# Performance work log

Measured on AMD Instinct MI355X. Metric: run time of the kernel, lower is better.

Reference implementation:

```python
import jax, jax.numpy as jnp
import numpy as np

EMBED_DIM = 1024
NUM_HEADS = 16
HEAD_DIM = EMBED_DIM // NUM_HEADS


def setup_inputs() -> dict:
    key = jax.random.key(0)
    kx, kq, kk, kv, ko = jax.random.split(key, 5)
    scale = 1.0 / np.sqrt(EMBED_DIM)
    return {
        "x": jax.random.normal(kx, (4, 2048, EMBED_DIM), dtype=jnp.float32),
        # nn.Linear weights are [out, in]; y = x @ W.T
        "w_q": jax.random.normal(kq, (EMBED_DIM, EMBED_DIM), dtype=jnp.float32) * scale,
        "w_k": jax.random.normal(kk, (EMBED_DIM, EMBED_DIM), dtype=jnp.float32) * scale,
        "w_v": jax.random.normal(kv, (EMBED_DIM, EMBED_DIM), dtype=jnp.float32) * scale,
        "w_o": jax.random.normal(ko, (EMBED_DIM, EMBED_DIM), dtype=jnp.float32) * scale,
    }


def reference(x, w_q, w_k, w_v, w_o):
    b, s, _ = x.shape
    # projections (Linear with no bias: x @ W.T)
    q = (x @ w_q.T).reshape(b, s, NUM_HEADS, HEAD_DIM).transpose(0, 2, 1, 3)
    k = (x @ w_k.T).reshape(b, s, NUM_HEADS, HEAD_DIM).transpose(0, 2, 1, 3)
    v = (x @ w_v.T).reshape(b, s, NUM_HEADS, HEAD_DIM).transpose(0, 2, 1, 3)
    # scores: [b, h, s, s]
    scores = jnp.einsum("bhqd,bhkd->bhqk", q, k) / jnp.sqrt(jnp.float32(HEAD_DIM)).astype(x.dtype)
    attn = jax.nn.softmax(scores, axis=-1)
    out = jnp.einsum("bhqk,bhkd->bhqd", attn, v)  # [b, h, s, d]
    out = out.transpose(0, 2, 1, 3).reshape(b, s, EMBED_DIM)
    return out @ w_o.T
```

## Files before the change

### kernel.cpp

```cpp
#include <hip/hip_runtime.h>
#include <math.h>

#define EMBED 1024
#define NHEAD 16
#define HDIM  64
#define BATCH 4
#define SEQ   2048
#define MROWS (BATCH * SEQ)

typedef __attribute__((ext_vector_type(4))) short short4v;
typedef __attribute__((ext_vector_type(8))) short short8;
typedef __attribute__((ext_vector_type(4))) float floatx4;
typedef __attribute__((ext_vector_type(16))) float floatx16;
typedef __attribute__((ext_vector_type(2))) unsigned uint2v;

#if __has_builtin(__builtin_amdgcn_exp2f)
#define EXP2(x) __builtin_amdgcn_exp2f(x)
#else
#define EXP2(x) exp2f(x)
#endif

__device__ __forceinline__ unsigned short f2bf(float f) {
  unsigned u = __float_as_uint(f);
  u += 0x7fffu + ((u >> 16) & 1u);
  return (unsigned short)(u >> 16);
}

#if __has_builtin(__builtin_amdgcn_cvt_pk_bf16_f32)
__device__ __forceinline__ unsigned pack2bf(float lo, float hi) {
  typedef __attribute__((ext_vector_type(2))) __bf16 bf2;
  union { bf2 b; unsigned u; } c;
  c.b = __builtin_amdgcn_cvt_pk_bf16_f32(lo, hi);
  return c.u;
}
#else
__device__ __forceinline__ unsigned pack2bf(float lo, float hi) {
  return ((__float_as_uint(lo) + 0x8000u) >> 16) |
         ((__float_as_uint(hi) + 0x8000u) & 0xffff0000u);
}
#endif

__device__ __forceinline__ uint2v pl32swap(unsigned a, unsigned b) {
#if __has_builtin(__builtin_amdgcn_permlane32_swap)
  return __builtin_amdgcn_permlane32_swap(a, b, false, false);
#else
  uint2v r;
  unsigned ax = (unsigned)__shfl_xor((int)a, 32);
  unsigned bx = (unsigned)__shfl_xor((int)b, 32);
  const int hi = (int)((threadIdx.x & 63) >> 5);
  r[0] = hi ? bx : a;
  r[1] = hi ? b : ax;
  return r;
#endif
}

__device__ __forceinline__ void gl_lds16(const void* g, void* l) {
  __builtin_amdgcn_global_load_lds(
      (const __attribute__((address_space(1))) unsigned int*)g,
      (__attribute__((address_space(3))) unsigned int*)l, 16, 0, 0);
}

__global__ __launch_bounds__(256) void cast_bf16_kernel(
    const float* __restrict__ x,  const float* __restrict__ wq,
    const float* __restrict__ wk, const float* __restrict__ wv,
    const float* __restrict__ wo,
    unsigned short* __restrict__ xb, unsigned short* __restrict__ wb) {
  const size_t NX = (size_t)MROWS * EMBED;
  size_t i4 = ((size_t)blockIdx.x * 256 + threadIdx.x) * 4;
  const float* src;
  unsigned short* dst;
  size_t off;
  if (i4 < NX) {
    src = x; dst = xb; off = i4;
  } else {
    size_t j = i4 - NX;
    int r = (int)(j >> 20);
    off = j & ((1u << 20) - 1);
    src = (r == 0) ? wq : (r == 1) ? wk : (r == 2) ? wv : wo;
    dst = wb + ((size_t)r << 20);
  }
  float4 v = *(const float4*)(src + off);
  ushort4 o;
  o.x = f2bf(v.x); o.y = f2bf(v.y); o.z = f2bf(v.z); o.w = f2bf(v.w);
  *(ushort4*)(dst + off) = o;
}

__device__ __forceinline__ void gemm_core(
    const unsigned short* __restrict__ Amat,
    const unsigned short* __restrict__ Bmat,
    int mBase, int nBase,
    unsigned short* As, unsigned short* Bs,
    floatx4 acc[4][4]) {
  const int t = threadIdx.x;
  const int lane = t & 63, w = t >> 6;
  const int wr = w >> 1, wc = w & 1;
  const int quad = lane >> 4, l15 = lane & 15;

  const int f0 = (w * 2 + 0) * 64 + lane;
  const int f1 = (w * 2 + 1) * 64 + lane;
  const unsigned short* ga0 = Amat + (size_t)(mBase + (f0 >> 2)) * EMBED + (f0 & 3) * 8;
  const unsigned short* ga1 = Amat + (size_t)(mBase + (f1 >> 2)) * EMBED + (f1 & 3) * 8;
  const unsigned short* gb0 = Bmat + (size_t)(nBase + (f0 >> 2)) * EMBED + (f0 & 3) * 8;
  const unsigned short* gb1 = Bmat + (size_t)(nBase + (f1 >> 2)) * EMBED + (f1 & 3) * 8;
  unsigned short* la0 = As + (w * 2 + 0) * 512;
  unsigned short* la1 = As + (w * 2 + 1) * 512;
  unsigned short* lb0 = Bs + (w * 2 + 0) * 512;
  unsigned short* lb1 = Bs + (w * 2 + 1) * 512;

  for (int kb = 0; kb < EMBED; kb += 32) {
    __syncthreads();
    gl_lds16(ga0 + kb, la0);
    gl_lds16(ga1 + kb, la1);
    gl_lds16(gb0 + kb, lb0);
    gl_lds16(gb1 + kb, lb1);
    __syncthreads();
    short8 a[4], b[4];
#pragma unroll
    for (int mi = 0; mi < 4; ++mi)
      a[mi] = *(const short8*)&As[(wr * 64 + mi * 16 + l15) * 32 + quad * 8];
#pragma unroll
    for (int ni = 0; ni < 4; ++ni)
      b[ni] = *(const short8*)&Bs[(wc * 64 + ni * 16 + l15) * 32 + quad * 8];
#pragma unroll
    for (int mi = 0; mi < 4; ++mi)
#pragma unroll
      for (int ni = 0; ni < 4; ++ni)
        acc[mi][ni] = __builtin_amdgcn_mfma_f32_16x16x32_bf16(
            a[mi], b[ni], acc[mi][ni], 0, 0, 0);
  }
}

__global__ __launch_bounds__(256) void proj_qkv_bf16(
    const unsigned short* __restrict__ xb,
    const unsigned short* __restrict__ wb,
    unsigned short* __restrict__ qkv) {
  const int id = blockIdx.x;
  const int xcd = id & 7;
  const int r = id >> 3;
  const int mn = r / 3;
  const int which = r - mn * 3;
  const int mBase = (xcd * 8 + (mn >> 3)) * 128;
  const int nBase = (mn & 7) * 128;

  const unsigned short* W = wb + ((size_t)which << 20);

  __shared__ unsigned short As[128 * 32];
  __shared__ unsigned short Bs[128 * 32];

  floatx4 acc[4][4] = {};
  gemm_core(xb, W, mBase, nBase, As, Bs, acc);

  const int t = threadIdx.x;
  const int lane = t & 63, w = t >> 6;
  const int wr = w >> 1, wc = w & 1;
  const int quad = lane >> 4, l15 = lane & 15;

  unsigned short* out = qkv + (size_t)which * MROWS * EMBED;
  if (which < 2) {
    const float scale = (which == 0) ? 0.18033688f : 1.0f;
#pragma unroll
    for (int mi = 0; mi < 4; ++mi)
#pragma unroll
      for (int ni = 0; ni < 4; ++ni) {
        const int n = nBase + wc * 64 + ni * 16 + l15;
        const int h = n >> 6, d = n & 63;
#pragma unroll
        for (int r2 = 0; r2 < 4; ++r2) {
          const int m = mBase + wr * 64 + mi * 16 + quad * 4 + r2;
          const int b = m >> 11, s = m & (SEQ - 1);
          out[(((size_t)(b * NHEAD + h) * SEQ) + s) * HDIM + d] =
              f2bf(acc[mi][ni][r2] * scale);
        }
      }
  } else {
#pragma unroll
    for (int mi = 0; mi < 4; ++mi) {
      const int m0 = mBase + wr * 64 + mi * 16 + quad * 4;
      const int b = m0 >> 11, s0 = m0 & (SEQ - 1);
#pragma unroll
      for (int ni = 0; ni < 4; ++ni) {
        const int n = nBase + wc * 64 + ni * 16 + l15;
        const int h = n >> 6, d = n & 63;
        ushort4 pk;
        pk.x = f2bf(acc[mi][ni][0]); pk.y = f2bf(acc[mi][ni][1]);
        pk.z = f2bf(acc[mi][ni][2]); pk.w = f2bf(acc[mi][ni][3]);
        *(ushort4*)&out[((size_t)(b * NHEAD + h) * HDIM + d) * SEQ + s0] = pk;
      }
    }
  }
}

__global__ __launch_bounds__(256, 2) void attn_mfma(
    const unsigned short* __restrict__ qkv,
    unsigned short* __restrict__ aout) {
  const unsigned short* Q = qkv;
  const unsigned short* K = qkv + (size_t)MROWS * EMBED;
  const unsigned short* V = qkv + 2 * (size_t)MROWS * EMBED;

  const int id = blockIdx.x;
  const int xcd = id & 7, slot = id >> 3;
  const int bh = xcd * 8 + (slot >> 3);
  const int qBase = (slot & 7) * 256;

  __shared__ unsigned short Ks[2 * 128 * 64];
  __shared__ unsigned short Vs[2 * 64 * 128];

  const int t = threadIdx.x;
  const int lane = t & 63, w = t >> 6;
  const int h2 = lane >> 5;
  const int q31 = lane & 31;

  const unsigned short* qrowA =
      Q + ((size_t)bh * SEQ + qBase + w * 64 + q31) * HDIM;
  const unsigned short* qrowB = qrowA + 32 * HDIM;
  short8 qaA[4], qaB[4];
#pragma unroll
  for (int ds = 0; ds < 4; ++ds) {
    qaA[ds] = *(const short8*)(qrowA + ds * 16 + h2 * 8);
    qaB[ds] = *(const short8*)(qrowB + ds * 16 + h2 * 8);
  }

  const unsigned short* kbase = K + (size_t)bh * SEQ * HDIM;
  const unsigned short* vbase = V + (size_t)bh * HDIM * SEQ;
  const unsigned short* gk[4];
  const unsigned short* gv[4];
  unsigned short* lk[4];
  unsigned short* lv[4];
#pragma unroll
  for (int i = 0; i < 4; ++i) {
    const int c = i * 256 + t;
    const int krow = c >> 3, kgrp = (c & 7) ^ (krow & 7);
    gk[i] = kbase + (size_t)krow * HDIM + kgrp * 8;
    const int vd = c >> 4, vj = (c & 15) ^ (vd & 15);
    gv[i] = vbase + (size_t)vd * SEQ + vj * 8;
    const int cu = i * 256 + w * 64;
    lk[i] = Ks + cu * 8;
    lv[i] = Vs + cu * 8;
  }

  floatx16 otA0 = {}, otA1 = {};
  floatx16 otB0 = {}, otB1 = {};
  float laccA = 0.0f, laccB = 0.0f;

#pragma unroll
  for (int i = 0; i < 4; ++i) {
    gl_lds16(gk[i], lk[i]);
    gl_lds16(gv[i], lv[i]);
  }

  for (int kt = 0; kt < SEQ; kt += 128) {
    const int cb = (kt >> 7) & 1;
    const int nb = cb ^ 1;
    const int nxt = (kt + 128) & (SEQ - 1);
    const int sOff = nb * 8192;
#pragma unroll
    for (int i = 0; i < 4; ++i) {
      gl_lds16(gk[i] + (size_t)nxt * HDIM, lk[i] + sOff);
      gl_lds16(gv[i] + nxt, lv[i] + sOff);
    }
    __builtin_amdgcn_sched_barrier(0);
    asm volatile("s_waitcnt vmcnt(8)" ::: "memory");
    __builtin_amdgcn_s_barrier();

    const int kOff = cb * 8192;
    const int vOff = cb * 8192;

#pragma unroll
    for (int sub = 0; sub < 2; ++sub) {
      const int koff = sub * 64;

      floatx16 stA0 = {}, stA1 = {}, stB0 = {}, stB1 = {};
      __builtin_amdgcn_s_setprio(1);
#pragma unroll
      for (int ds = 0; ds < 4; ++ds) {
        const int g = ds * 2 + h2;
        const int k0 = koff + q31;
        short8 ka0 = *(const short8*)&Ks[kOff + k0 * 64 + ((g ^ (q31 & 7)) * 8)];
        stA0 = __builtin_amdgcn_mfma_f32_32x32x16_bf16(ka0, qaA[ds], stA0, 0, 0, 0);
        stB0 = __builtin_amdgcn_mfma_f32_32x32x16_bf16(ka0, qaB[ds], stB0, 0, 0, 0);
        const int k1 = koff + 32 + q31;
        short8 ka1 = *(const short8*)&Ks[kOff + k1 * 64 + ((g ^ (q31 & 7)) * 8)];
        stA1 = __builtin_amdgcn_mfma_f32_32x32x16_bf16(ka1, qaA[ds], stA1, 0, 0, 0);
        stB1 = __builtin_amdgcn_mfma_f32_32x32x16_bf16(ka1, qaB[ds], stB1, 0, 0, 0);
      }
      __builtin_amdgcn_s_setprio(0);

      unsigned pkA0[8], pkA1[8], pkB0[8], pkB1[8];
#pragma unroll
      for (int i = 0; i < 8; ++i) {
        float a0 = EXP2(stA0[2 * i]), b0 = EXP2(stA0[2 * i + 1]);
        float a1 = EXP2(stA1[2 * i]), b1 = EXP2(stA1[2 * i + 1]);
        laccA += (a0 + b0) + (a1 + b1);
        pkA0[i] = pack2bf(a0, b0);
        pkA1[i] = pack2bf(a1, b1);
        float c0 = EXP2(stB0[2 * i]), d0 = EXP2(stB0[2 * i + 1]);
        float c1 = EXP2(stB1[2 * i]), d1 = EXP2(stB1[2 * i + 1]);
        laccB += (c0 + d0) + (c1 + d1);
        pkB0[i] = pack2bf(c0, d0);
        pkB1[i] = pack2bf(c1, d1);
      }

      __builtin_amdgcn_s_setprio(1);
#pragma unroll
      for (int sp = 0; sp < 4; ++sp) {
        const unsigned* pA = (sp < 2) ? pkA0 : pkA1;
        const unsigned* pB = (sp < 2) ? pkB0 : pkB1;
        const int off = (sp & 1) * 4;
        uint2v ra0 = pl32swap(pA[off + 0], pA[off + 2]);
        uint2v ra1 = pl32swap(pA[off + 1], pA[off + 3]);
        uint2v rb0 = pl32swap(pB[off + 0], pB[off + 2]);
        uint2v rb1 = pl32swap(pB[off + 1], pB[off + 3]);
        union { unsigned u[4]; short8 v; } pbA, pbB;
        pbA.u[0] = ra0[0]; pbA.u[1] = ra1[0]; pbA.u[2] = ra0[1]; pbA.u[3] = ra1[1];
        pbB.u[0] = rb0[0]; pbB.u[1] = rb1[0]; pbB.u[2] = rb0[1]; pbB.u[3] = rb1[1];

        const int g8 = sub * 8 + sp * 2 + h2;
        const int pos = (g8 ^ (q31 & 15)) * 8;
        short8 va0 = *(const short8*)&Vs[vOff + q31 * 128 + pos];
        otA0 = __builtin_amdgcn_mfma_f32_32x32x16_bf16(va0, pbA.v, otA0, 0, 0, 0);
        otB0 = __builtin_amdgcn_mfma_f32_32x32x16_bf16(va0, pbB.v, otB0, 0, 0, 0);
        short8 va1 = *(const short8*)&Vs[vOff + (32 + q31) * 128 + pos];
        otA1 = __builtin_amdgcn_mfma_f32_32x32x16_bf16(va1, pbA.v, otA1, 0, 0, 0);
        otB1 = __builtin_amdgcn_mfma_f32_32x32x16_bf16(va1, pbB.v, otB1, 0, 0, 0);
      }
      __builtin_amdgcn_s_setprio(0);
    }

    __builtin_amdgcn_sched_barrier(0);
    __builtin_amdgcn_s_barrier();
  }
  asm volatile("s_waitcnt vmcnt(0)" ::: "memory");

  const float totA = laccA + __shfl_xor(laccA, 32);
  const float totB = laccB + __shfl_xor(laccB, 32);
  const float invA = 1.0f / totA;
  const float invB = 1.0f / totB;

  const int b = bh >> 4, hh = bh & 15;
  unsigned short* orowA =
      aout + ((size_t)b * SEQ + qBase + w * 64 + q31) * EMBED + hh * HDIM;
  unsigned short* orowB = orowA + (size_t)32 * EMBED;
#pragma unroll
  for (int rg = 0; rg < 4; ++rg) {
    const int d0 = rg * 8 + h2 * 4;
    ushort4 p0, p1;
    p0.x = f2bf(otA0[4 * rg + 0] * invA); p0.y = f2bf(otA0[4 * rg + 1] * invA);
    p0.z = f2bf(otA0[4 * rg + 2] * invA); p0.w = f2bf(otA0[4 * rg + 3] * invA);
    *(ushort4*)(orowA + d0) = p0;
    p1.x = f2bf(otA1[4 * rg + 0] * invA); p1.y = f2bf(otA1[4 * rg + 1] * invA);
    p1.z = f2bf(otA1[4 * rg + 2] * invA); p1.w = f2bf(otA1[4 * rg + 3] * invA);
    *(ushort4*)(orowA + 32 + d0) = p1;
    ushort4 p2, p3;
    p2.x = f2bf(otB0[4 * rg + 0] * invB); p2.y = f2bf(otB0[4 * rg + 1] * invB);
    p2.z = f2bf(otB0[4 * rg + 2] * invB); p2.w = f2bf(otB0[4 * rg + 3] * invB);
    *(ushort4*)(orowB + d0) = p2;
    p3.x = f2bf(otB1[4 * rg + 0] * invB); p3.y = f2bf(otB1[4 * rg + 1] * invB);
    p3.z = f2bf(otB1[4 * rg + 2] * invB); p3.w = f2bf(otB1[4 * rg + 3] * invB);
    *(ushort4*)(orowB + 32 + d0) = p3;
  }
}

__global__ __launch_bounds__(256) void out_proj_bf16(
    const unsigned short* __restrict__ aout,
    const unsigned short* __restrict__ wb,
    float* __restrict__ Cout) {
  const int id = blockIdx.x;
  const int xcd = id & 7;
  const int r = id >> 3;
  const int mBase = (xcd * 8 + (r >> 3)) * 128;
  const int nBase = (r & 7) * 128;

  __shared__ unsigned short As[128 * 32];
  __shared__ unsigned short Bs[128 * 32];

  floatx4 acc[4][4] = {};
  gemm_core(aout, wb + ((size_t)3 << 20), mBase, nBase, As, Bs, acc);

  const int t = threadIdx.x;
  const int lane = t & 63, w = t >> 6;
  const int wr = w >> 1, wc = w & 1;
  const int quad = lane >> 4, l15 = lane & 15;

#pragma unroll
  for (int mi = 0; mi < 4; ++mi)
#pragma unroll
    for (int ni = 0; ni < 4; ++ni) {
      const int n = nBase + wc * 64 + ni * 16 + l15;
#pragma unroll
      for (int r2 = 0; r2 < 4; ++r2) {
        const int m = mBase + wr * 64 + mi * 16 + quad * 4 + r2;
        Cout[(size_t)m * EMBED + n] = acc[mi][ni][r2];
      }
    }
}

extern "C" void kernel_launch(void* const* d_in, const int* in_sizes, int n_in,
                              void* d_out, int out_size, void* d_ws, size_t ws_size,
                              hipStream_t stream) {
  const float* x  = (const float*)d_in[0];
  const float* wq = (const float*)d_in[1];
  const float* wk = (const float*)d_in[2];
  const float* wv = (const float*)d_in[3];
  const float* wo = (const float*)d_in[4];
  float* out = (float*)d_out;

  char* ws = (char*)d_ws;
  unsigned short* xb   = (unsigned short*)(ws);
  unsigned short* wb   = (unsigned short*)(ws + (16u << 20));
  unsigned short* qkv  = (unsigned short*)(ws + (26u << 20));
  unsigned short* aout = (unsigned short*)(ws + (76u << 20));

  cast_bf16_kernel<<<12288, 256, 0, stream>>>(x, wq, wk, wv, wo, xb, wb);
  proj_qkv_bf16<<<1536, 256, 0, stream>>>(xb, wb, qkv);
  attn_mfma<<<512, 256, 0, stream>>>(qkv, aout);
  out_proj_bf16<<<512, 256, 0, stream>>>(aout, wb, out);
}
```

Baseline: 273.0 us.

## Rewrite projection GEMMs with 256x256 tiles, swizzled LDS and pipelined prefetch

Replaces the 128x128 single-buffered GEMM core with a 256x256-tile, 512-thread core that uses 64-wide K steps, XOR-swizzled LDS layout, and double-buffered direct global-to-LDS loads interleaved with MFMA phases via explicit waitcnt, barriers and setprio. QKV projection now treats the three weights as one N=3072 matrix, and out-projection uses 128 large blocks. The goal is to raise arithmetic intensity, avoid LDS bank conflicts and hide load latency in the projection GEMMs. The cost is 128KB LDS per block and fewer blocks (128 for out_proj), which may underfill the 256 CUs.

```diff
diff --git a/kernel.cpp b/kernel.cpp
--- a/kernel.cpp
+++ b/kernel.cpp
@@ -85,88 +85,152 @@
   *(ushort4*)(dst + off) = o;
 }
 
-__device__ __forceinline__ void gemm_core(
+#define RD_A(bo, mi, ks) (*(const short8*)&LA[(bo) + wr * 8192 + \
+    ((mi) * 16 + l15) * 64 + ((((ks) * 4 + quad) ^ (l15 & 7)) * 8)])
+#define RD_B(bo, ni, ks) (*(const short8*)&LB[(bo) + hB * 8192 + \
+    (rB0 + (ni) * 16 + l15) * 64 + ((((ks) * 4 + quad) ^ (l15 & 7)) * 8)])
+
+__device__ __forceinline__ void gemm_core8(
     const unsigned short* __restrict__ Amat,
     const unsigned short* __restrict__ Bmat,
     int mBase, int nBase,
-    unsigned short* As, unsigned short* Bs,
-    floatx4 acc[4][4]) {
+    unsigned short* LA, unsigned short* LB,
+    floatx4 acc[8][4]) {
   const int t = threadIdx.x;
-  const int lane = t & 63, w = t >> 6;
-  const int wr = w >> 1, wc = w & 1;
+  const int lane = t & 63, wv = t >> 6;
+  const int wr = wv >> 2, wc = wv & 3;
   const int quad = lane >> 4, l15 = lane & 15;
-
-  const int f0 = (w * 2 + 0) * 64 + lane;
-  const int f1 = (w * 2 + 1) * 64 + lane;
-  const unsigned short* ga0 = Amat + (size_t)(mBase + (f0 >> 2)) * EMBED + (f0 & 3) * 8;
-  const unsigned short* ga1 = Amat + (size_t)(mBase + (f1 >> 2)) * EMBED + (f1 & 3) * 8;
-  const unsigned short* gb0 = Bmat + (size_t)(nBase + (f0 >> 2)) * EMBED + (f0 & 3) * 8;
-  const unsigned short* gb1 = Bmat + (size_t)(nBase + (f1 >> 2)) * EMBED + (f1 & 3) * 8;
-  unsigned short* la0 = As + (w * 2 + 0) * 512;
-  unsigned short* la1 = As + (w * 2 + 1) * 512;
-  unsigned short* lb0 = Bs + (w * 2 + 0) * 512;
-  unsigned short* lb1 = Bs + (w * 2 + 1) * 512;
-
-  for (int kb = 0; kb < EMBED; kb += 32) {
-    __syncthreads();
-    gl_lds16(ga0 + kb, la0);
-    gl_lds16(ga1 + kb, la1);
-    gl_lds16(gb0 + kb, lb0);
-    gl_lds16(gb1 + kb, lb1);
-    __syncthreads();
-    short8 a[4], b[4];
-#pragma unroll
-    for (int mi = 0; mi < 4; ++mi)
-      a[mi] = *(const short8*)&As[(wr * 64 + mi * 16 + l15) * 32 + quad * 8];
-#pragma unroll
-    for (int ni = 0; ni < 4; ++ni)
-      b[ni] = *(const short8*)&Bs[(wc * 64 + ni * 16 + l15) * 32 + quad * 8];
-#pragma unroll
-    for (int mi = 0; mi < 4; ++mi)
-#pragma unroll
-      for (int ni = 0; ni < 4; ++ni)
-        acc[mi][ni] = __builtin_amdgcn_mfma_f32_16x16x32_bf16(
-            a[mi], b[ni], acc[mi][ni], 0, 0, 0);
-  }
-}
-
-__global__ __launch_bounds__(256) void proj_qkv_bf16(
+  const int hB = wc >> 1, rB0 = (wc & 1) * 64;
+
+  const unsigned short* sA[2][2];
+  const unsigned short* sB[2][2];
+  unsigned short* dA[2][2];
+  unsigned short* dB[2][2];
+#pragma unroll
+  for (int h = 0; h < 2; ++h)
+#pragma unroll
+    for (int i = 0; i < 2; ++i) {
+      const int c = i * 512 + t;
+      const int row = c >> 3, g = (c & 7) ^ (row & 7);
+      sA[h][i] = Amat + (size_t)(mBase + h * 128 + row) * EMBED + g * 8;
+      sB[h][i] = Bmat + (size_t)(nBase + h * 128 + row) * EMBED + g * 8;
+      const int du = h * 8192 + (i * 512 + wv * 64) * 8;
+      dA[h][i] = LA + du;
+      dB[h][i] = LB + du;
+    }
+
+  gl_lds16(sA[0][0], dA[0][0]); gl_lds16(sA[0][1], dA[0][1]);
+  gl_lds16(sA[1][0], dA[1][0]); gl_lds16(sA[1][1], dA[1][1]);
+  gl_lds16(sB[0][0], dB[0][0]); gl_lds16(sB[0][1], dB[0][1]);
+  gl_lds16(sB[1][0], dB[1][0]); gl_lds16(sB[1][1], dB[1][1]);
+  gl_lds16(sB[0][0] + 64, dB[0][0] + 16384);
+  gl_lds16(sB[0][1] + 64, dB[0][1] + 16384);
+  gl_lds16(sB[1][0] + 64, dB[1][0] + 16384);
+  gl_lds16(sB[1][1] + 64, dB[1][1] + 16384);
+
+  short8 b[4][2];
+  for (int T = 0; T < 16; T += 2) {
+#pragma unroll
+    for (int hf = 0; hf < 2; ++hf) {
+      const int bo = hf * 16384;
+#pragma unroll
+      for (int p = 0; p < 4; ++p) {
+        short8 a[2][2];
+        if (p == 0) {
+          {
+            const int ts = (T + 1 + hf) & 15, tb = (ts & 1) * 16384;
+            gl_lds16(sA[0][0] + (size_t)ts * 64, dA[0][0] + tb);
+            gl_lds16(sA[0][1] + (size_t)ts * 64, dA[0][1] + tb);
+          }
+          asm volatile("s_waitcnt vmcnt(6)" ::: "memory");
+          __builtin_amdgcn_sched_barrier(0);
+          __builtin_amdgcn_s_barrier();
+#pragma unroll
+          for (int ni = 0; ni < 4; ++ni) {
+            b[ni][0] = RD_B(bo, ni, 0);
+            b[ni][1] = RD_B(bo, ni, 1);
+          }
+          a[0][0] = RD_A(bo, 0, 0); a[0][1] = RD_A(bo, 0, 1);
+          a[1][0] = RD_A(bo, 1, 0); a[1][1] = RD_A(bo, 1, 1);
+        } else {
+          const int mi0 = 2 * p;
+          a[0][0] = RD_A(bo, mi0, 0);     a[0][1] = RD_A(bo, mi0, 1);
+          a[1][0] = RD_A(bo, mi0 + 1, 0); a[1][1] = RD_A(bo, mi0 + 1, 1);
+          if (p == 1) {
+            const int ts = (T + 1 + hf) & 15, tb = (ts & 1) * 16384;
+            gl_lds16(sA[1][0] + (size_t)ts * 64, dA[1][0] + tb);
+            gl_lds16(sA[1][1] + (size_t)ts * 64, dA[1][1] + tb);
+          } else if (p == 2) {
+            const int ts = (T + 2 + hf) & 15, tb = (ts & 1) * 16384;
+            gl_lds16(sB[0][0] + (size_t)ts * 64, dB[0][0] + tb);
+            gl_lds16(sB[0][1] + (size_t)ts * 64, dB[0][1] + tb);
+          } else {
+            const int ts = (T + 2 + hf) & 15, tb = (ts & 1) * 16384;
+            gl_lds16(sB[1][0] + (size_t)ts * 64, dB[1][0] + tb);
+            gl_lds16(sB[1][1] + (size_t)ts * 64, dB[1][1] + tb);
+          }
+          __builtin_amdgcn_sched_barrier(0);
+          __builtin_amdgcn_s_barrier();
+        }
+        asm volatile("s_waitcnt lgkmcnt(0)" ::: "memory");
+        __builtin_amdgcn_sched_barrier(0);
+        __builtin_amdgcn_s_setprio(1);
+        const int mi0 = 2 * p;
+#pragma unroll
+        for (int m2 = 0; m2 < 2; ++m2)
+#pragma unroll
+          for (int ni = 0; ni < 4; ++ni) {
+            acc[mi0 + m2][ni] = __builtin_amdgcn_mfma_f32_16x16x32_bf16(
+                a[m2][0], b[ni][0], acc[mi0 + m2][ni], 0, 0, 0);
+            acc[mi0 + m2][ni] = __builtin_amdgcn_mfma_f32_16x16x32_bf16(
+                a[m2][1], b[ni][1], acc[mi0 + m2][ni], 0, 0, 0);
+          }
+        __builtin_amdgcn_s_setprio(0);
+        __builtin_amdgcn_sched_barrier(0);
+        __builtin_amdgcn_s_barrier();
+      }
+    }
+  }
+  asm volatile("s_waitcnt vmcnt(0)" ::: "memory");
+}
+
+__global__ __launch_bounds__(512, 2) void proj_qkv_bf16(
     const unsigned short* __restrict__ xb,
     const unsigned short* __restrict__ wb,
     unsigned short* __restrict__ qkv) {
   const int id = blockIdx.x;
   const int xcd = id & 7;
   const int r = id >> 3;
-  const int mn = r / 3;
-  const int which = r - mn * 3;
-  const int mBase = (xcd * 8 + (mn >> 3)) * 128;
-  const int nBase = (mn & 7) * 128;
-
-  const unsigned short* W = wb + ((size_t)which << 20);
-
-  __shared__ unsigned short As[128 * 32];
-  __shared__ unsigned short Bs[128 * 32];
-
-  floatx4 acc[4][4] = {};
-  gemm_core(xb, W, mBase, nBase, As, Bs, acc);
+  const int nIdx = r >> 2;
+  const int mBase = (xcd * 4 + (r & 3)) * 256;
+  const int nBase = nIdx * 256;
+
+  __shared__ unsigned short LA[32768];
+  __shared__ unsigned short LB[32768];
+
+  floatx4 acc[8][4] = {};
+  gemm_core8(xb, wb, mBase, nBase, LA, LB, acc);
 
   const int t = threadIdx.x;
-  const int lane = t & 63, w = t >> 6;
-  const int wr = w >> 1, wc = w & 1;
+  const int lane = t & 63, wv = t >> 6;
+  const int wr = wv >> 2, wc = wv & 3;
   const int quad = lane >> 4, l15 = lane & 15;
 
+  const int which = nBase >> 10;
+  const int nloc0 = nBase & 1023;
   unsigned short* out = qkv + (size_t)which * MROWS * EMBED;
+
   if (which < 2) {
     const float scale = (which == 0) ? 0.18033688f : 1.0f;
 #pragma unroll
-    for (int mi = 0; mi < 4; ++mi)
+    for (int mi = 0; mi < 8; ++mi)
 #pragma unroll
       for (int ni = 0; ni < 4; ++ni) {
-        const int n = nBase + wc * 64 + ni * 16 + l15;
-        const int h = n >> 6, d = n & 63;
+        const int nn = nloc0 + wc * 64 + ni * 16 + l15;
+        const int h = nn >> 6, d = nn & 63;
 #pragma unroll
         for (int r2 = 0; r2 < 4; ++r2) {
-          const int m = mBase + wr * 64 + mi * 16 + quad * 4 + r2;
+          const int m = mBase + wr * 128 + mi * 16 + quad * 4 + r2;
           const int b = m >> 11, s = m & (SEQ - 1);
           out[(((size_t)(b * NHEAD + h) * SEQ) + s) * HDIM + d] =
               f2bf(acc[mi][ni][r2] * scale);
@@ -174,13 +238,13 @@
       }
   } else {
 #pragma unroll
-    for (int mi = 0; mi < 4; ++mi) {
-      const int m0 = mBase + wr * 64 + mi * 16 + quad * 4;
+    for (int mi = 0; mi < 8; ++mi) {
+      const int m0 = mBase + wr * 128 + mi * 16 + quad * 4;
       const int b = m0 >> 11, s0 = m0 & (SEQ - 1);
 #pragma unroll
       for (int ni = 0; ni < 4; ++ni) {
-        const int n = nBase + wc * 64 + ni * 16 + l15;
-        const int h = n >> 6, d = n & 63;
+        const int nn = nloc0 + wc * 64 + ni * 16 + l15;
+        const int h = nn >> 6, d = nn & 63;
         ushort4 pk;
         pk.x = f2bf(acc[mi][ni][0]); pk.y = f2bf(acc[mi][ni][1]);
         pk.z = f2bf(acc[mi][ni][2]); pk.w = f2bf(acc[mi][ni][3]);
@@ -360,35 +424,35 @@
   }
 }
 
-__global__ __launch_bounds__(256) void out_proj_bf16(
+__global__ __launch_bounds__(512, 2) void out_proj_bf16(
     const unsigned short* __restrict__ aout,
     const unsigned short* __restrict__ wb,
     float* __restrict__ Cout) {
   const int id = blockIdx.x;
   const int xcd = id & 7;
   const int r = id >> 3;
-  const int mBase = (xcd * 8 + (r >> 3)) * 128;
-  const int nBase = (r & 7) * 128;
-
-  __shared__ unsigned short As[128 * 32];
-  __shared__ unsigned short Bs[128 * 32];
-
-  floatx4 acc[4][4] = {};
-  gemm_core(aout, wb + ((size_t)3 << 20), mBase, nBase, As, Bs, acc);
+  const int nBase = (r >> 2) * 256;
+  const int mBase = (xcd * 4 + (r & 3)) * 256;
+
+  __shared__ unsigned short LA[32768];
+  __shared__ unsigned short LB[32768];
+
+  floatx4 acc[8][4] = {};
+  gemm_core8(aout, wb + ((size_t)3 << 20), mBase, nBase, LA, LB, acc);
 
   const int t = threadIdx.x;
-  const int lane = t & 63, w = t >> 6;
-  const int wr = w >> 1, wc = w & 1;
+  const int lane = t & 63, wv = t >> 6;
+  const int wr = wv >> 2, wc = wv & 3;
   const int quad = lane >> 4, l15 = lane & 15;
 
 #pragma unroll
-  for (int mi = 0; mi < 4; ++mi)
+  for (int mi = 0; mi < 8; ++mi)
 #pragma unroll
     for (int ni = 0; ni < 4; ++ni) {
       const int n = nBase + wc * 64 + ni * 16 + l15;
 #pragma unroll
       for (int r2 = 0; r2 < 4; ++r2) {
-        const int m = mBase + wr * 64 + mi * 16 + quad * 4 + r2;
+        const int m = mBase + wr * 128 + mi * 16 + quad * 4 + r2;
         Cout[(size_t)m * EMBED + n] = acc[mi][ni][r2];
       }
     }
@@ -411,7 +475,7 @@
   unsigned short* aout = (unsigned short*)(ws + (76u << 20));
 
   cast_bf16_kernel<<<12288, 256, 0, stream>>>(x, wq, wk, wv, wo, xb, wb);
-  proj_qkv_bf16<<<1536, 256, 0, stream>>>(xb, wb, qkv);
+  proj_qkv_bf16<<<384, 512, 0, stream>>>(xb, wb, qkv);
   attn_mfma<<<512, 256, 0, stream>>>(qkv, aout);
-  out_proj_bf16<<<512, 256, 0, stream>>>(aout, wb, out);
-}
+  out_proj_bf16<<<128, 512, 0, stream>>>(aout, wb, out);
+}
```

New measurement: 272.1 us. Within noise of the previous version (-0.3%).
